# Performance work log

Measured on AMD Instinct MI355X. Metric: run time of the kernel, lower is better.

Reference implementation:

```python
import jax, jax.numpy as jnp
import numpy as np

N = 8192; E = 131072; K = 20; IN_DIM = 3; HID = 256; N_CLASSES = 32


def setup_inputs():
    key = jax.random.key(0)
    ks = jax.random.split(key, 16)

    def w(k, shape):
        lim = 1.0 / np.sqrt(shape[0])
        return jax.random.uniform(k, shape, jnp.float32, -lim, lim)

    f32 = jnp.float32
    return {
        "features": jax.random.normal(ks[0], (N, IN_DIM), f32),
        "src": jax.random.randint(ks[1], (E,), 0, N, jnp.int32),
        "dst": jax.random.randint(ks[2], (E,), 0, N, jnp.int32),
        # GraphConv params
        "Wc1": w(ks[3], (IN_DIM, HID)), "bc1": jnp.zeros((HID,), f32),
        "Wc2": w(ks[4], (HID, HID)), "bc2": jnp.zeros((HID,), f32),
        "Wc3": w(ks[5], (64, N_CLASSES)), "bc3": jnp.zeros((N_CLASSES,), f32),
        # DynamicEdgeConv 1 MLP: [2*256 -> 256 -> 256], Linear+BN+ReLU each
        "W11": w(ks[6], (2 * HID, 256)), "b11": jnp.zeros((256,), f32), "g11": jnp.ones((256,), f32), "be11": jnp.zeros((256,), f32),
        "W12": w(ks[7], (256, 256)), "b12": jnp.zeros((256,), f32), "g12": jnp.ones((256,), f32), "be12": jnp.zeros((256,), f32),
        # DynamicEdgeConv 2 MLP: [2*256 -> 64 -> 64]
        "W21": w(ks[8], (2 * 256, 64)), "b21": jnp.zeros((64,), f32), "g21": jnp.ones((64,), f32), "be21": jnp.zeros((64,), f32),
        "W22": w(ks[9], (64, 64)), "b22": jnp.zeros((64,), f32), "g22": jnp.ones((64,), f32), "be22": jnp.zeros((64,), f32),
    }


def reference(features, src, dst, Wc1, bc1, Wc2, bc2, Wc3, bc3,
              W11, b11, g11, be11, W12, b12, g12, be12,
              W21, b21, g21, be21, W22, b22, g22, be22):
    n = features.shape[0]
    ones_e = jnp.ones(src.shape[0], features.dtype)
    # DGL GraphConv norm='both': deg clamped to min 1
    dout = jnp.clip(jax.ops.segment_sum(ones_e, src, num_segments=n), 1.0) ** -0.5
    din = jnp.clip(jax.ops.segment_sum(ones_e, dst, num_segments=n), 1.0) ** -0.5

    def gconv(x, W, b, act):
        agg = jax.ops.segment_sum((x * dout[:, None])[src], dst, num_segments=n)
        r = (agg * din[:, None]) @ W + b
        return jax.nn.relu(r) if act else r

    def bn(x, g, b):  # BatchNorm1d in training mode over all edge rows
        mu = jnp.mean(x, axis=(0, 1), keepdims=True)
        var = jnp.mean(jnp.square(x - mu), axis=(0, 1), keepdims=True)
        return (x - mu) * jax.lax.rsqrt(var + 1e-5) * g + b

    def edge_conv(x, layers):
        # dynamic kNN graph on current features (self included, dist 0)
        sq = jnp.sum(x * x, axis=-1)
        d = sq[:, None] + sq[None, :] - 2.0 * (x @ x.T)  # [N,N]
        idx = jax.lax.top_k(-d, K)[1]                    # [N,K]
        xi = x[:, None, :]
        e = jnp.concatenate([jnp.broadcast_to(xi, (n, K, x.shape[-1])), x[idx] - xi], axis=-1)  # [N,K,2F]
        for W, b, g, be in layers:
            e = jax.nn.relu(bn(e @ W + b, g, be))
        return jnp.max(e, axis=1)  # max aggregation over neighbors

    h = gconv(features, Wc1, bc1, True)                                   # [N,256]
    h = edge_conv(h, [(W11, b11, g11, be11), (W12, b12, g12, be12)])      # [N,256]
    h = gconv(h, Wc2, bc2, True)                                          # [N,256]
    h = edge_conv(h, [(W21, b21, g21, be21), (W22, b22, g22, be22)])      # [N,64]
    return gconv(h, Wc3, bc3, False)                                      # [N,32]
```

## Files before the change

### kernel.cpp

```cpp
#include <hip/hip_runtime.h>

#define NN 8192
#define NE 131072
#define KNN 20
#define CH 4096
#define GBM 128
#define GBN 128
#define GBK 64

typedef __attribute__((ext_vector_type(4))) float f32x4;
typedef __attribute__((ext_vector_type(8))) __bf16 bf16x8;

__global__ void k_zero(float* p, int n){
  int i = blockIdx.x*256 + threadIdx.x;
  if (i < n) p[i] = 0.f;
}
__global__ void k_zero_i(int* p, int n){
  int i = blockIdx.x*256 + threadIdx.x;
  if (i < n) p[i] = 0;
}

__device__ __forceinline__ unsigned short f2bf(float x){
  unsigned u = __float_as_uint(x);
  unsigned r = (u + 0x7fff + ((u >> 16) & 1)) >> 16;
  return (unsigned short)r;
}
__device__ __forceinline__ float bf2f(unsigned short h){
  return __uint_as_float((unsigned)h << 16);
}
__device__ __forceinline__ void gload16(const void* g, void* l){
  __builtin_amdgcn_global_load_lds(
      (const __attribute__((address_space(1))) void*)g,
      (__attribute__((address_space(3))) void*)l, 16, 0, 0);
}

__global__ void k_count(const int* __restrict__ src, const int* __restrict__ dst,
                        int* cs, int* cd){
  int e = blockIdx.x*256 + threadIdx.x;
  if (e < NE){ atomicAdd(&cs[src[e]], 1); atomicAdd(&cd[dst[e]], 1); }
}
__global__ void k_deg(const int* cs, const int* cd, float* dout, float* din){
  int i = blockIdx.x*256 + threadIdx.x;
  if (i < NN){
    dout[i] = rsqrtf((float)max(cs[i], 1));
    din[i]  = rsqrtf((float)max(cd[i], 1));
  }
}
__global__ void k_scan(const int* __restrict__ cnt, int* __restrict__ off){
  __shared__ int sh[256];
  __shared__ int carry;
  int tid = threadIdx.x;
  if (tid == 0) carry = 0;
  __syncthreads();
  for (int base = 0; base < NN; base += 256){
    int v = cnt[base + tid];
    int x = v;
    sh[tid] = x; __syncthreads();
    for (int o = 1; o < 256; o <<= 1){
      int y = (tid >= o) ? sh[tid - o] : 0;
      __syncthreads();
      x += y; sh[tid] = x;
      __syncthreads();
    }
    off[base + tid] = carry + x - v;
    __syncthreads();
    if (tid == 255){
      carry += x;
      if (base + 256 == NN) off[NN] = carry;
    }
    __syncthreads();
  }
}
__global__ void k_fill(const int* __restrict__ src, const int* __restrict__ dst,
                       const int* __restrict__ roff, int* cursor, int* csr){
  int e = blockIdx.x*256 + threadIdx.x;
  if (e < NE){
    int d = dst[e];
    int p = atomicAdd(&cursor[d], 1);
    csr[roff[d] + p] = src[e];
  }
}

__global__ void k_gconv1(const float* __restrict__ feat, const int* __restrict__ roff,
                         const int* __restrict__ csr, const float* __restrict__ dout,
                         const float* __restrict__ din, const float* __restrict__ Wc1,
                         const float* __restrict__ bc1, float* __restrict__ h1){
  int wid = threadIdx.x >> 6, lane = threadIdx.x & 63;
  int i = blockIdx.x*4 + wid;
  float a0=0.f, a1=0.f, a2=0.f;
  int beg = roff[i], end = roff[i+1];
  for (int t = beg + lane; t < end; t += 64){
    int s = csr[t]; float w = dout[s];
    a0 += feat[s*3+0]*w; a1 += feat[s*3+1]*w; a2 += feat[s*3+2]*w;
  }
  for (int m = 32; m; m >>= 1){
    a0 += __shfl_xor(a0, m); a1 += __shfl_xor(a1, m); a2 += __shfl_xor(a2, m);
  }
  float dn = din[i];
  a0 *= dn; a1 *= dn; a2 *= dn;
  for (int c = lane; c < 256; c += 64){
    float r = a0*Wc1[c] + a1*Wc1[256+c] + a2*Wc1[512+c] + bc1[c];
    h1[(size_t)i*256 + c] = fmaxf(r, 0.f);
  }
}

__global__ void k_sq(const float* __restrict__ X, float* __restrict__ sq){
  int wid = threadIdx.x >> 6, lane = threadIdx.x & 63;
  int i = blockIdx.x*4 + wid;
  float4 v = *(const float4*)&X[(size_t)i*256 + lane*4];
  float s = v.x*v.x + v.y*v.y + v.z*v.z + v.w*v.w;
  for (int m = 32; m; m >>= 1) s += __shfl_xor(s, m);
  if (lane == 0) sq[i] = s;
}

__global__ void k_split(const float* __restrict__ X, unsigned short* __restrict__ xcat){
  int row = blockIdx.x, c = threadIdx.x;
  float x = X[(size_t)row*256 + c];
  unsigned short h = f2bf(x);
  unsigned short lo = f2bf(x - bf2f(h));
  xcat[(size_t)row*512 + c] = h;
  xcat[(size_t)row*512 + 256 + c] = lo;
}

__global__ void k_wsplit(const float* __restrict__ W, unsigned short* __restrict__ Whi,
                         unsigned short* __restrict__ Wlo){
  int k = blockIdx.x, n = threadIdx.x;
  float x = W[(size_t)k*256 + n];
  unsigned short h = f2bf(x);
  Whi[(size_t)n*256 + k] = h;
  Wlo[(size_t)n*256 + k] = f2bf(x - bf2f(h));
}

__global__ __launch_bounds__(256)
void k_gram_mfma(const unsigned short* __restrict__ Xcat,
                 float* __restrict__ G, int r0){
  __shared__ unsigned short sA[GBM*GBK];
  __shared__ unsigned short sB[GBM*GBK];
  int tid = threadIdx.x;
  int lw = tid >> 6, l = tid & 63;
  int rbl = blockIdx.y*GBM;
  int rb = r0 + rbl;
  int cb = blockIdx.x*GBN;

  int srow = l >> 3;
  int scol = (l & 7) ^ srow;
  const unsigned short* srcA[4];
  const unsigned short* srcB[4];
  char* dstA[4]; char* dstB[4];
  #pragma unroll
  for (int i = 0; i < 4; i++){
    int c = lw*4 + i;
    int row = c*8 + srow;
    srcA[i] = Xcat + (size_t)(rb + row)*512 + scol*8;
    srcB[i] = Xcat + (size_t)(cb + row)*512 + scol*8;
    dstA[i] = (char*)sA + c*1024;
    dstB[i] = (char*)sB + c*1024;
  }

  int wm = lw >> 1, wn = lw & 1;
  int fm = l & 15, kg = l >> 4;
  unsigned offA[4][2], offB[4][2];
  #pragma unroll
  for (int mf = 0; mf < 4; mf++){
    int rowa = wm*64 + mf*16 + fm;
    int rowb = wn*64 + mf*16 + fm;
    #pragma unroll
    for (int ks = 0; ks < 2; ks++){
      offA[mf][ks] = rowa*128 + (((unsigned)(ks*4 + kg) ^ (rowa & 7)))*16;
      offB[mf][ks] = rowb*128 + (((unsigned)(ks*4 + kg) ^ (rowb & 7)))*16;
    }
  }

  f32x4 acc[4][4];
  #pragma unroll
  for (int m = 0; m < 4; m++)
    #pragma unroll
    for (int n = 0; n < 4; n++) acc[m][n] = (f32x4){0.f,0.f,0.f,0.f};

  #pragma unroll
  for (int s = 0; s < 12; s++){
    int sec = s >> 2;
    int inner = (s & 3)*64;
    int cbA = (sec == 1 ? 256 : 0) + inner;
    int cbB = (sec == 2 ? 256 : 0) + inner;
    #pragma unroll
    for (int i = 0; i < 4; i++){
      gload16(srcA[i] + cbA, dstA[i]);
      gload16(srcB[i] + cbB, dstB[i]);
    }
    __syncthreads();
    #pragma unroll
    for (int ks = 0; ks < 2; ks++){
      bf16x8 a[4], b[4];
      #pragma unroll
      for (int mf = 0; mf < 4; mf++) a[mf] = *(const bf16x8*)((const char*)sA + offA[mf][ks]);
      #pragma unroll
      for (int nf = 0; nf < 4; nf++) b[nf] = *(const bf16x8*)((const char*)sB + offB[nf][ks]);
      #pragma unroll
      for (int mf = 0; mf < 4; mf++)
        #pragma unroll
        for (int nf = 0; nf < 4; nf++)
          acc[mf][nf] = __builtin_amdgcn_mfma_f32_16x16x32_bf16(a[mf], b[nf], acc[mf][nf], 0, 0, 0);
    }
    __syncthreads();
  }

  #pragma unroll
  for (int mf = 0; mf < 4; mf++){
    int orow = rbl + wm*64 + mf*16 + kg*4;
    #pragma unroll
    for (int nf = 0; nf < 4; nf++){
      int ocol = cb + wn*64 + nf*16 + fm;
      #pragma unroll
      for (int r = 0; r < 4; r++)
        G[(size_t)(orow + r)*NN + ocol] = acc[mf][nf][r];
    }
  }
}

__global__ __launch_bounds__(256)
void k_topk(const float* __restrict__ G, const float* __restrict__ sq,
            int r0, int* __restrict__ idxo){
  __shared__ float lsq[NN];
  int tid = threadIdx.x;
  for (int t = tid; t < NN/4; t += 256)
    ((float4*)lsq)[t] = ((const float4*)sq)[t];
  __syncthreads();

  int wid = tid >> 6, lane = tid & 63;
  int rl = blockIdx.x*4 + wid;
  int gr = r0 + rl;
  const float4* row4 = (const float4*)(G + (size_t)rl*NN);
  const float4* lsq4 = (const float4*)lsq;
  float sqr = lsq[gr];

  float kd0=INFINITY,kd1=INFINITY,kd2=INFINITY,kd3=INFINITY,kd4=INFINITY,
        kd5=INFINITY,kd6=INFINITY,kd7=INFINITY,kd8=INFINITY,kd9=INFINITY,
        kd10=INFINITY,kd11=INFINITY,kd12=INFINITY,kd13=INFINITY,kd14=INFINITY,
        kd15=INFINITY,kd16=INFINITY,kd17=INFINITY,kd18=INFINITY,kd19=INFINITY;
  int ki0=0x7fffffff,ki1=0x7fffffff,ki2=0x7fffffff,ki3=0x7fffffff,ki4=0x7fffffff,
      ki5=0x7fffffff,ki6=0x7fffffff,ki7=0x7fffffff,ki8=0x7fffffff,ki9=0x7fffffff,
      ki10=0x7fffffff,ki11=0x7fffffff,ki12=0x7fffffff,ki13=0x7fffffff,ki14=0x7fffffff,
      ki15=0x7fffffff,ki16=0x7fffffff,ki17=0x7fffffff,ki18=0x7fffffff,ki19=0x7fffffff;

#define ST(U) { bool sw = nk < kd##U; float tv = kd##U; int tq = ki##U; \
      if (sw){ kd##U = nk; ki##U = ni; nk = tv; ni = tq; } }
#define INSE(kc, jc) { if ((kc) < kd19){ float nk = (kc); int ni = (jc); \
      ST(0) ST(1) ST(2) ST(3) ST(4) ST(5) ST(6) ST(7) ST(8) ST(9) \
      ST(10) ST(11) ST(12) ST(13) ST(14) ST(15) ST(16) ST(17) ST(18) ST(19) } }

  #pragma unroll 1
  for (int o = 0; o < 32; o++){
    int t4 = lane + o*64;
    float4 g = row4[t4];
    float4 s = lsq4[t4];
    int jb = t4*4;
    float k0 = (sqr + s.x) - 2.f*g.x;
    float k1 = (sqr + s.y) - 2.f*g.y;
    float k2 = (sqr + s.z) - 2.f*g.z;
    float k3 = (sqr + s.w) - 2.f*g.w;
    float t19 = kd19;
    float mn = fminf(fminf(k0,k1), fminf(k2,k3));
    if (__any(mn < t19)){
      INSE(k0, jb+0);
      INSE(k1, jb+1);
      INSE(k2, jb+2);
      INSE(k3, jb+3);
    }
  }
#undef INSE
#undef ST

#define MV(A,B) { kd##A = kd##B; ki##A = ki##B; }
  #pragma unroll 1
  for (int r = 0; r < KNN; r++){
    float bv = kd0; int bi = ki0;
    #pragma unroll
    for (int mm = 32; mm; mm >>= 1){
      float ov = __shfl_xor(bv, mm); int oi = __shfl_xor(bi, mm);
      if (ov < bv || (ov == bv && oi < bi)){ bv = ov; bi = oi; }
    }
    if (ki0 == bi){
      MV(0,1) MV(1,2) MV(2,3) MV(3,4) MV(4,5) MV(5,6) MV(6,7) MV(7,8) MV(8,9) MV(9,10)
      MV(10,11) MV(11,12) MV(12,13) MV(13,14) MV(14,15) MV(15,16) MV(16,17) MV(17,18) MV(18,19)
      kd19 = INFINITY; ki19 = 0x7fffffff;
    }
    if (lane == 0) idxo[(size_t)gr*KNN + r] = bi;
  }
#undef MV
}

__global__ void k_wd(const float* __restrict__ W, float* __restrict__ Wd, int rows, int M){
  int t = blockIdx.x*256 + threadIdx.x;
  if (t < rows*M) Wd[t] = W[t] - W[rows*M + t];
}

__global__ __launch_bounds__(256)
void k_mm(const float* __restrict__ A, const float* __restrict__ B,
          const float* __restrict__ bias, float* __restrict__ Cout,
          int n, int Kd, int M, int relu){
  __shared__ float la[16][68], lb[16][68];
  int tid = threadIdx.x;
  int rb = blockIdx.y*64, cb = blockIdx.x*64;
  int lr = tid >> 2, lq = (tid & 3)*4;
  int ty = tid >> 4, tx = tid & 15;
  float acc[4][4] = {};
  for (int k0 = 0; k0 < Kd; k0 += 16){
    __syncthreads();
    #pragma unroll
    for (int u = 0; u < 4; u++){
      int k = k0 + lq + u;
      la[lq+u][lr] = (k < Kd) ? A[(size_t)(rb+lr)*Kd + k] : 0.f;
    }
    int kk = tid >> 4; int cc = (tid & 15)*4;
    #pragma unroll
    for (int u = 0; u < 4; u++){
      int c = cb + cc + u; int k = k0 + kk;
      lb[kk][cc+u] = (k < Kd && c < M) ? B[(size_t)k*M + c] : 0.f;
    }
    __syncthreads();
    #pragma unroll
    for (int k = 0; k < 16; k++){
      float4 a = *(const float4*)&la[k][ty*4];
      float4 b = *(const float4*)&lb[k][tx*4];
      float avv[4] = {a.x,a.y,a.z,a.w}, bvv[4] = {b.x,b.y,b.z,b.w};
      #pragma unroll
      for (int u = 0; u < 4; u++)
        #pragma unroll
        for (int v = 0; v < 4; v++) acc[u][v] += avv[u]*bvv[v];
    }
  }
  #pragma unroll
  for (int u = 0; u < 4; u++){
    int r = rb + ty*4 + u;
    #pragma unroll
    for (int v = 0; v < 4; v++){
      int c = cb + tx*4 + v;
      if (c < M){
        float x = acc[u][v] + (bias ? bias[c] : 0.f);
        if (relu) x = fmaxf(x, 0.f);
        Cout[(size_t)r*M + c] = x;
      }
    }
  }
}

template<int C>
__global__ __launch_bounds__(256)
void k_stats1(const float* __restrict__ A, const float* __restrict__ P,
              const int* __restrict__ idx, float* __restrict__ ssum, float* __restrict__ ssq){
  __shared__ int si[128], sj[128];
  int tid = threadIdx.x;
  int s0 = blockIdx.x*128;
  if (tid < 128){ si[tid] = (s0 + tid)/KNN; sj[tid] = idx[s0 + tid]; }
  __syncthreads();
  constexpr int MPAR = 256/C;
  int tc = tid % C, sr = tid / C;
  float s = 0.f, q = 0.f;
  for (int m = sr; m < 128; m += MPAR){
    float v = A[(size_t)si[m]*C + tc] + P[(size_t)sj[m]*C + tc];
    s += v; q += v*v;
  }
  if constexpr (MPAR > 1){
    __shared__ float rs[256], rq[256];
    rs[tid] = s; rq[tid] = q; __syncthreads();
    if (sr == 0){
      for (int u = 1; u < MPAR; u++){ s += rs[u*C + tc]; q += rq[u*C + tc]; }
    }
  }
  if (sr == 0){ atomicAdd(&ssum[tc], s); atomicAdd(&ssq[tc], q); }
}

template<int C>
__global__ __launch_bounds__(256)
void k_colstats(const float* __restrict__ X, float* __restrict__ ssum, float* __restrict__ ssq){
  constexpr int MPAR = 256/C;
  int tid = threadIdx.x;
  int tc = tid % C, sr = tid / C;
  int base = blockIdx.x*256;
  float s = 0.f, q = 0.f;
  for (int m = sr; m < 256; m += MPAR){
    float v = X[(size_t)(base + m)*C + tc];
    s += v; q += v*v;
  }
  if constexpr (MPAR > 1){
    __shared__ float rs[256], rq[256];
    rs[tid] = s; rq[tid] = q; __syncthreads();
    if (sr == 0){
      for (int u = 1; u < MPAR; u++){ s += rs[u*C + tc]; q += rq[u*C + tc]; }
    }
  }
  if (sr == 0){ atomicAdd(&ssum[tc], s); atomicAdd(&ssq[tc], q); }
}

__global__ void k_bn_final(const float* __restrict__ ssum, const float* __restrict__ ssq,
                           const float* __restrict__ g, const float* __restrict__ be,
                           float* __restrict__ sb, float* __restrict__ tb, int C, float invn){
  int c = threadIdx.x;
  if (c < C){
    float mu = ssum[c]*invn;
    float var = fmaxf(ssq[c]*invn - mu*mu, 0.f);
    float s = g[c]*rsqrtf(var + 1e-5f);
    sb[c] = s; tb[c] = be[c] - mu*s;
  }
}

__global__ __launch_bounds__(256, 2)
void k_edge_mfma(const float* __restrict__ A, const float* __restrict__ P,
                 const int* __restrict__ idx, const float* __restrict__ sb,
                 const float* __restrict__ tb, const unsigned short* __restrict__ Wthi,
                 const unsigned short* __restrict__ Wtlo, const float* __restrict__ bias,
                 float* __restrict__ out){
  __shared__ unsigned short ehi[64*256];
  __shared__ unsigned short elo[64*256];
  __shared__ int sj[64];
  int tid = threadIdx.x;
  int lw = tid >> 6, l = tid & 63;
  int s0 = blockIdx.x*64;
  if (tid < 64) sj[tid] = idx[s0 + tid];
  float sbc = sb[tid], tbc = tb[tid];
  __syncthreads();

  #pragma unroll 1
  for (int it = 0; it < 64; it++){
    int i = (s0 + it)/KNN;
    int j = sj[it];
    float v = (A[(size_t)i*256 + tid] + P[(size_t)j*256 + tid])*sbc + tbc;
    v = fmaxf(v, 0.f);
    unsigned short h = f2bf(v);
    unsigned short lo = f2bf(v - bf2f(h));
    unsigned off = (unsigned)it*512 + (((unsigned)tid*2) ^ (((unsigned)it & 7) << 4));
    *(unsigned short*)((char*)ehi + off) = h;
    *(unsigned short*)((char*)elo + off) = lo;
  }
  __syncthreads();

  int fm = l & 15, kg = l >> 4;
  const unsigned short* bhi[4];
  const unsigned short* blo[4];
  float bz[4];
  #pragma unroll
  for (int nf = 0; nf < 4; nf++){
    int col = lw*64 + nf*16 + fm;
    bhi[nf] = Wthi + (size_t)col*256 + kg*8;
    blo[nf] = Wtlo + (size_t)col*256 + kg*8;
    bz[nf] = bias[col];
  }

  f32x4 acc[4][4];
  #pragma unroll
  for (int m = 0; m < 4; m++)
    #pragma unroll
    for (int n = 0; n < 4; n++) acc[m][n] = (f32x4){0.f,0.f,0.f,0.f};

  #pragma unroll 1
  for (int sec = 0; sec < 3; sec++){
    const char* abase = (sec == 1) ? (const char*)elo : (const char*)ehi;
    int bsec = (sec == 2);
    #pragma unroll 1
    for (int st = 0; st < 8; st++){
      int g = st*4 + kg;
      bf16x8 a[4], b[4];
      #pragma unroll
      for (int mf = 0; mf < 4; mf++){
        int row = mf*16 + fm;
        a[mf] = *(const bf16x8*)(abase + row*512 + ((unsigned)(g ^ (row & 7)))*16);
      }
      #pragma unroll
      for (int nf = 0; nf < 4; nf++){
        const unsigned short* bp = bsec ? blo[nf] : bhi[nf];
        b[nf] = *(const bf16x8*)(bp + st*32);
      }
      #pragma unroll
      for (int mf = 0; mf < 4; mf++)
        #pragma unroll
        for (int nf = 0; nf < 4; nf++)
          acc[mf][nf] = __builtin_amdgcn_mfma_f32_16x16x32_bf16(a[mf], b[nf], acc[mf][nf], 0, 0, 0);
    }
  }

  #pragma unroll
  for (int mf = 0; mf < 4; mf++){
    #pragma unroll
    for (int nf = 0; nf < 4; nf++){
      int col = lw*64 + nf*16 + fm;
      #pragma unroll
      for (int r = 0; r < 4; r++){
        int row = s0 + mf*16 + kg*4 + r;
        out[(size_t)row*256 + col] = acc[mf][nf][r] + bz[nf];
      }
    }
  }
}

template<int C>
__global__ __launch_bounds__(256)
void k_edge_mm(const float* __restrict__ A, const float* __restrict__ P,
               const int* __restrict__ idx, const float* __restrict__ sb,
               const float* __restrict__ tb, const float* __restrict__ W,
               const float* __restrict__ bias, float* __restrict__ out){
  constexpr int BM   = (C == 256) ? 32 : 64;
  constexpr int KT   = (C == 256) ? 16 : 64;
  constexpr int COLG = C/8;
  constexpr int ROWG = 256/COLG;
  constexpr int EPT  = BM/ROWG;
  constexpr int MPAR = 256/C;
  __shared__ float e2[BM][C+1];
  __shared__ float wt[KT][C+4];
  __shared__ int sj[BM];
  int tid = threadIdx.x;
  int s0 = blockIdx.x*BM;
  if (tid < BM) sj[tid] = idx[s0 + tid];
  __syncthreads();
  for (int mb = 0; mb < BM; mb += MPAR){
    int m = mb + tid / C;
    int c = tid % C;
    int i = (s0 + m)/KNN;
    int j = sj[m];
    float v = (A[(size_t)i*C + c] + P[(size_t)j*C + c])*sb[c] + tb[c];
    e2[m][c] = fmaxf(v, 0.f);
  }
  float acc[EPT][8];
  #pragma unroll
  for (int m = 0; m < EPT; m++)
    #pragma unroll
    for (int u = 0; u < 8; u++) acc[m][u] = 0.f;
  int tr = tid / COLG, tc = tid % COLG;
  for (int kt = 0; kt < C; kt += KT){
    __syncthreads();
    for (int t = tid; t < KT*C; t += 256){
      wt[t / C][t % C] = W[(size_t)(kt + t/C)*C + (t % C)];
    }
    __syncthreads();
    #pragma unroll 4
    for (int k = 0; k < KT; k++){
      float4 w0 = *(const float4*)&wt[k][tc*8];
      float4 w1 = *(const float4*)&wt[k][tc*8 + 4];
      float b[8] = {w0.x,w0.y,w0.z,w0.w,w1.x,w1.y,w1.z,w1.w};
      #pragma unroll
      for (int m = 0; m < EPT; m++){
        float a = e2[tr*EPT + m][kt + k];
        #pragma unroll
        for (int u = 0; u < 8; u++) acc[m][u] += a*b[u];
      }
    }
  }
  #pragma unroll
  for (int m = 0; m < EPT; m++){
    int row = s0 + tr*EPT + m;
    float4 o0, o1;
    o0.x = acc[m][0] + bias[tc*8+0]; o0.y = acc[m][1] + bias[tc*8+1];
    o0.z = acc[m][2] + bias[tc*8+2]; o0.w = acc[m][3] + bias[tc*8+3];
    o1.x = acc[m][4] + bias[tc*8+4]; o1.y = acc[m][5] + bias[tc*8+5];
    o1.z = acc[m][6] + bias[tc*8+6]; o1.w = acc[m][7] + bias[tc*8+7];
    *(float4*)&out[(size_t)row*C + tc*8]     = o0;
    *(float4*)&out[(size_t)row*C + tc*8 + 4] = o1;
  }
}

template<int C>
__global__ void k_maxpool(const float* __restrict__ X, const float* __restrict__ sb,
                          const float* __restrict__ tb, float* __restrict__ H){
  constexpr int NPB = 256/C;
  int node = blockIdx.x*NPB + threadIdx.x / C;
  int c = threadIdx.x % C;
  float s = sb[c], t = tb[c];
  float mx = 0.f;
  for (int k = 0; k < KNN; k++){
    float v = X[(size_t)(node*KNN + k)*C + c]*s + t;
    mx = fmaxf(mx, v);
  }
  H[(size_t)node*C + c] = mx;
}

template<int C>
__global__ void k_agg(const float* __restrict__ X, const int* __restrict__ roff,
                      const int* __restrict__ csr, const float* __restrict__ dout,
                      const float* __restrict__ din, float* __restrict__ XA){
  int i = blockIdx.x; int c = threadIdx.x;
  float acc = 0.f;
  int b = roff[i], e = roff[i+1];
  for (int t = b; t < e; t++){
    int s = csr[t];
    acc += X[(size_t)s*C + c]*dout[s];
  }
  XA[(size_t)i*C + c] = acc*din[i];
}

extern "C" void kernel_launch(void* const* d_in, const int* in_sizes, int n_in,
                              void* d_out, int out_size, void* d_ws, size_t ws_size,
                              hipStream_t stream){
  const float* feat = (const float*)d_in[0];
  const int*   src  = (const int*)d_in[1];
  const int*   dst  = (const int*)d_in[2];
  const float* Wc1  = (const float*)d_in[3];
  const float* bc1  = (const float*)d_in[4];
  const float* Wc2  = (const float*)d_in[5];
  const float* bc2  = (const float*)d_in[6];
  const float* Wc3  = (const float*)d_in[7];
  const float* bc3  = (const float*)d_in[8];
  const float* W11  = (const float*)d_in[9];
  const float* b11  = (const float*)d_in[10];
  const float* g11  = (const float*)d_in[11];
  const float* be11 = (const float*)d_in[12];
  const float* W12  = (const float*)d_in[13];
  const float* b12  = (const float*)d_in[14];
  const float* g12  = (const float*)d_in[15];
  const float* be12 = (const float*)d_in[16];
  const float* W21  = (const float*)d_in[17];
  const float* b21  = (const float*)d_in[18];
  const float* g21  = (const float*)d_in[19];
  const float* be21 = (const float*)d_in[20];
  const float* W22  = (const float*)d_in[21];
  const float* b22  = (const float*)d_in[22];
  const float* g22  = (const float*)d_in[23];
  const float* be22 = (const float*)d_in[24];
  float* out = (float*)d_out;

  char* w = (char*)d_ws; size_t off = 0;
  auto alloc = [&](size_t bytes)->void*{
    void* p = w + off;
    off += bytes; off = (off + 255) & ~(size_t)255;
    return p;
  };
  int* cnt_s  = (int*)alloc(NN*4);
  int* cnt_d  = (int*)alloc(NN*4);
  int* roff   = (int*)alloc((NN+1)*4);
  int* cursor = (int*)alloc(NN*4);
  int* csr    = (int*)alloc(NE*4);
  int* idx    = (int*)alloc((size_t)NN*KNN*4);
  float* dout = (float*)alloc(NN*4);
  float* din  = (float*)alloc(NN*4);
  float* sqv  = (float*)alloc(NN*4);
  float* h1   = (float*)alloc((size_t)NN*256*4);
  float* h2   = (float*)alloc((size_t)NN*256*4);
  float* h3   = (float*)alloc((size_t)NN*256*4);
  float* h4   = (float*)alloc((size_t)NN*64*4);
  float* xa   = (float*)alloc((size_t)NN*256*4);
  float* Abuf = (float*)alloc((size_t)NN*256*4);
  float* Pbuf = (float*)alloc((size_t)NN*256*4);
  float* Wd   = (float*)alloc(256*256*4);
  float* ssum = (float*)alloc(256*4);
  float* ssq  = (float*)alloc(256*4);
  float* sbn  = (float*)alloc(256*4);
  float* tbn  = (float*)alloc(256*4);
  unsigned short* wthi = (unsigned short*)alloc(256*256*2);
  unsigned short* wtlo = (unsigned short*)alloc(256*256*2);
  float* out2 = (float*)alloc((size_t)NN*KNN*256*4);
  float* gram = out2;
  unsigned short* xcat = (unsigned short*)(out2 + (size_t)CH*NN);
  (void)ws_size; (void)n_in; (void)in_sizes; (void)out_size;

  const float invn = 1.0f / (float)(NN*KNN);

  k_zero_i<<<32, 256, 0, stream>>>(cnt_s, NN);
  k_zero_i<<<32, 256, 0, stream>>>(cnt_d, NN);
  k_zero_i<<<32, 256, 0, stream>>>(cursor, NN);
  k_count<<<NE/256, 256, 0, stream>>>(src, dst, cnt_s, cnt_d);
  k_deg<<<32, 256, 0, stream>>>(cnt_s, cnt_d, dout, din);
  k_scan<<<1, 256, 0, stream>>>(cnt_d, roff);
  k_fill<<<NE/256, 256, 0, stream>>>(src, dst, roff, cursor, csr);

  k_gconv1<<<NN/4, 256, 0, stream>>>(feat, roff, csr, dout, din, Wc1, bc1, h1);

  k_sq<<<NN/4, 256, 0, stream>>>(h1, sqv);
  k_split<<<NN, 256, 0, stream>>>(h1, xcat);
  for (int r0 = 0; r0 < NN; r0 += CH){
    k_gram_mfma<<<dim3(NN/GBN, CH/GBM), 256, 0, stream>>>(xcat, gram, r0);
    k_topk<<<CH/4, 256, 0, stream>>>(gram, sqv, r0, idx);
  }
  k_wd<<<256, 256, 0, stream>>>(W11, Wd, 256, 256);
  k_wsplit<<<256, 256, 0, stream>>>(W12, wthi, wtlo);
  k_mm<<<dim3(4, NN/64), 256, 0, stream>>>(h1, Wd, b11, Abuf, NN, 256, 256, 0);
  k_mm<<<dim3(4, NN/64), 256, 0, stream>>>(h1, W11 + 256*256, nullptr, Pbuf, NN, 256, 256, 0);
  k_zero<<<2, 256, 0, stream>>>(ssum, 256); k_zero<<<2, 256, 0, stream>>>(ssq, 256);
  k_stats1<256><<<NN*KNN/128, 256, 0, stream>>>(Abuf, Pbuf, idx, ssum, ssq);
  k_bn_final<<<1, 256, 0, stream>>>(ssum, ssq, g11, be11, sbn, tbn, 256, invn);
  k_edge_mfma<<<NN*KNN/64, 256, 0, stream>>>(Abuf, Pbuf, idx, sbn, tbn, wthi, wtlo, b12, out2);
  k_zero<<<2, 256, 0, stream>>>(ssum, 256); k_zero<<<2, 256, 0, stream>>>(ssq, 256);
  k_colstats<256><<<NN*KNN/256, 256, 0, stream>>>(out2, ssum, ssq);
  k_bn_final<<<1, 256, 0, stream>>>(ssum, ssq, g12, be12, sbn, tbn, 256, invn);
  k_maxpool<256><<<NN, 256, 0, stream>>>(out2, sbn, tbn, h2);

  k_agg<256><<<NN, 256, 0, stream>>>(h2, roff, csr, dout, din, xa);
  k_mm<<<dim3(4, NN/64), 256, 0, stream>>>(xa, Wc2, bc2, h3, NN, 256, 256, 1);

  k_sq<<<NN/4, 256, 0, stream>>>(h3, sqv);
  k_split<<<NN, 256, 0, stream>>>(h3, xcat);
  for (int r0 = 0; r0 < NN; r0 += CH){
    k_gram_mfma<<<dim3(NN/GBN, CH/GBM), 256, 0, stream>>>(xcat, gram, r0);
    k_topk<<<CH/4, 256, 0, stream>>>(gram, sqv, r0, idx);
  }
  k_wd<<<64, 256, 0, stream>>>(W21, Wd, 256, 64);
  k_mm<<<dim3(1, NN/64), 256, 0, stream>>>(h3, Wd, b21, Abuf, NN, 256, 64, 0);
  k_mm<<<dim3(1, NN/64), 256, 0, stream>>>(h3, W21 + 256*64, nullptr, Pbuf, NN, 256, 64, 0);
  k_zero<<<2, 256, 0, stream>>>(ssum, 256); k_zero<<<2, 256, 0, stream>>>(ssq, 256);
  k_stats1<64><<<NN*KNN/128, 256, 0, stream>>>(Abuf, Pbuf, idx, ssum, ssq);
  k_bn_final<<<1, 256, 0, stream>>>(ssum, ssq, g21, be21, sbn, tbn, 64, invn);
  k_edge_mm<64><<<NN*KNN/64, 256, 0, stream>>>(Abuf, Pbuf, idx, sbn, tbn, W22, b22, out2);
  k_zero<<<2, 256, 0, stream>>>(ssum, 256); k_zero<<<2, 256, 0, stream>>>(ssq, 256);
  k_colstats<64><<<NN*KNN/256, 256, 0, stream>>>(out2, ssum, ssq);
  k_bn_final<<<1, 256, 0, stream>>>(ssum, ssq, g22, be22, sbn, tbn, 64, invn);
  k_maxpool<64><<<NN/4, 256, 0, stream>>>(out2, sbn, tbn, h4);

  k_agg<64><<<NN, 64, 0, stream>>>(h4, roff, csr, dout, din, xa);
  k_mm<<<dim3(1, NN/64), 256, 0, stream>>>(xa, Wc3, bc3, out, NN, 64, 32, 0);
}
```

Measured before the change: 1.462 ms.

## Fuse BN column stats into edge GEMMs and move 64-wide edge MLP to MFMA

```diff
diff --git a/kernel.cpp b/kernel.cpp
--- a/kernel.cpp
+++ b/kernel.cpp
@@ -130,6 +130,14 @@
   Whi[(size_t)n*256 + k] = h;
   Wlo[(size_t)n*256 + k] = f2bf(x - bf2f(h));
 }
+__global__ void k_wsplit64(const float* __restrict__ W, unsigned short* __restrict__ Whi,
+                           unsigned short* __restrict__ Wlo){
+  int k = blockIdx.x, n = threadIdx.x;
+  float x = W[(size_t)k*64 + n];
+  unsigned short h = f2bf(x);
+  Whi[(size_t)n*64 + k] = h;
+  Wlo[(size_t)n*64 + k] = f2bf(x - bf2f(h));
+}
 
 __global__ __launch_bounds__(256)
 void k_gram_mfma(const unsigned short* __restrict__ Xcat,
@@ -249,12 +257,16 @@
       ST(0) ST(1) ST(2) ST(3) ST(4) ST(5) ST(6) ST(7) ST(8) ST(9) \
       ST(10) ST(11) ST(12) ST(13) ST(14) ST(15) ST(16) ST(17) ST(18) ST(19) } }
 
+  float4 gc = row4[lane];
+  float4 sc = lsq4[lane];
   #pragma unroll 1
   for (int o = 0; o < 32; o++){
-    int t4 = lane + o*64;
-    float4 g = row4[t4];
-    float4 s = lsq4[t4];
-    int jb = t4*4;
+    float4 g = gc, s = sc;
+    if (o < 31){
+      gc = row4[lane + (o+1)*64];
+      sc = lsq4[lane + (o+1)*64];
+    }
+    int jb = (lane + o*64)*4;
     float k0 = (sqr + s.x) - 2.f*g.x;
     float k1 = (sqr + s.y) - 2.f*g.y;
     float k2 = (sqr + s.z) - 2.f*g.z;
@@ -371,28 +383,6 @@
   if (sr == 0){ atomicAdd(&ssum[tc], s); atomicAdd(&ssq[tc], q); }
 }
 
-template<int C>
-__global__ __launch_bounds__(256)
-void k_colstats(const float* __restrict__ X, float* __restrict__ ssum, float* __restrict__ ssq){
-  constexpr int MPAR = 256/C;
-  int tid = threadIdx.x;
-  int tc = tid % C, sr = tid / C;
-  int base = blockIdx.x*256;
-  float s = 0.f, q = 0.f;
-  for (int m = sr; m < 256; m += MPAR){
-    float v = X[(size_t)(base + m)*C + tc];
-    s += v; q += v*v;
-  }
-  if constexpr (MPAR > 1){
-    __shared__ float rs[256], rq[256];
-    rs[tid] = s; rq[tid] = q; __syncthreads();
-    if (sr == 0){
-      for (int u = 1; u < MPAR; u++){ s += rs[u*C + tc]; q += rq[u*C + tc]; }
-    }
-  }
-  if (sr == 0){ atomicAdd(&ssum[tc], s); atomicAdd(&ssq[tc], q); }
-}
-
 __global__ void k_bn_final(const float* __restrict__ ssum, const float* __restrict__ ssq,
                            const float* __restrict__ g, const float* __restrict__ be,
                            float* __restrict__ sb, float* __restrict__ tb, int C, float invn){
@@ -410,7 +400,7 @@
                  const int* __restrict__ idx, const float* __restrict__ sb,
                  const float* __restrict__ tb, const unsigned short* __restrict__ Wthi,
                  const unsigned short* __restrict__ Wtlo, const float* __restrict__ bias,
-                 float* __restrict__ out){
+                 float* __restrict__ out, float* __restrict__ ssum, float* __restrict__ ssq){
   __shared__ unsigned short ehi[64*256];
   __shared__ unsigned short elo[64*256];
   __shared__ int sj[64];
@@ -422,16 +412,25 @@
   __syncthreads();
 
   #pragma unroll 1
-  for (int it = 0; it < 64; it++){
-    int i = (s0 + it)/KNN;
-    int j = sj[it];
-    float v = (A[(size_t)i*256 + tid] + P[(size_t)j*256 + tid])*sbc + tbc;
-    v = fmaxf(v, 0.f);
-    unsigned short h = f2bf(v);
-    unsigned short lo = f2bf(v - bf2f(h));
-    unsigned off = (unsigned)it*512 + (((unsigned)tid*2) ^ (((unsigned)it & 7) << 4));
-    *(unsigned short*)((char*)ehi + off) = h;
-    *(unsigned short*)((char*)elo + off) = lo;
+  for (int g = 0; g < 8; g++){
+    float va[8];
+    #pragma unroll
+    for (int u = 0; u < 8; u++){
+      int it = g*8 + u;
+      int i = (s0 + it)/KNN;
+      int j = sj[it];
+      va[u] = A[(size_t)i*256 + tid] + P[(size_t)j*256 + tid];
+    }
+    #pragma unroll
+    for (int u = 0; u < 8; u++){
+      int it = g*8 + u;
+      float v = fmaxf(va[u]*sbc + tbc, 0.f);
+      unsigned short h = f2bf(v);
+      unsigned short lo = f2bf(v - bf2f(h));
+      unsigned off = (unsigned)it*512 + (((unsigned)tid*2) ^ (((unsigned)it & 7) << 4));
+      *(unsigned short*)((char*)ehi + off) = h;
+      *(unsigned short*)((char*)elo + off) = lo;
+    }
   }
   __syncthreads();
 
@@ -479,6 +478,9 @@
     }
   }
 
+  float s4[4], q4[4];
+  #pragma unroll
+  for (int nf = 0; nf < 4; nf++){ s4[nf] = 0.f; q4[nf] = 0.f; }
   #pragma unroll
   for (int mf = 0; mf < 4; mf++){
     #pragma unroll
@@ -487,74 +489,141 @@
       #pragma unroll
       for (int r = 0; r < 4; r++){
         int row = s0 + mf*16 + kg*4 + r;
-        out[(size_t)row*256 + col] = acc[mf][nf][r] + bz[nf];
+        float v = acc[mf][nf][r] + bz[nf];
+        out[(size_t)row*256 + col] = v;
+        s4[nf] += v; q4[nf] += v*v;
       }
     }
   }
-}
-
-template<int C>
-__global__ __launch_bounds__(256)
-void k_edge_mm(const float* __restrict__ A, const float* __restrict__ P,
-               const int* __restrict__ idx, const float* __restrict__ sb,
-               const float* __restrict__ tb, const float* __restrict__ W,
-               const float* __restrict__ bias, float* __restrict__ out){
-  constexpr int BM   = (C == 256) ? 32 : 64;
-  constexpr int KT   = (C == 256) ? 16 : 64;
-  constexpr int COLG = C/8;
-  constexpr int ROWG = 256/COLG;
-  constexpr int EPT  = BM/ROWG;
-  constexpr int MPAR = 256/C;
-  __shared__ float e2[BM][C+1];
-  __shared__ float wt[KT][C+4];
-  __shared__ int sj[BM];
+  #pragma unroll
+  for (int nf = 0; nf < 4; nf++){
+    s4[nf] += __shfl_xor(s4[nf], 16); q4[nf] += __shfl_xor(q4[nf], 16);
+    s4[nf] += __shfl_xor(s4[nf], 32); q4[nf] += __shfl_xor(q4[nf], 32);
+  }
+  if (kg == 0){
+    #pragma unroll
+    for (int nf = 0; nf < 4; nf++){
+      int col = lw*64 + nf*16 + fm;
+      atomicAdd(&ssum[col], s4[nf]);
+      atomicAdd(&ssq[col], q4[nf]);
+    }
+  }
+}
+
+__global__ __launch_bounds__(256, 2)
+void k_edge_mfma64(const float* __restrict__ A, const float* __restrict__ P,
+                   const int* __restrict__ idx, const float* __restrict__ sb,
+                   const float* __restrict__ tb, const unsigned short* __restrict__ Wthi,
+                   const unsigned short* __restrict__ Wtlo, const float* __restrict__ bias,
+                   float* __restrict__ out, float* __restrict__ ssum, float* __restrict__ ssq){
+  __shared__ unsigned short ehi[128*64];
+  __shared__ unsigned short elo[128*64];
+  __shared__ int sj[128];
   int tid = threadIdx.x;
-  int s0 = blockIdx.x*BM;
-  if (tid < BM) sj[tid] = idx[s0 + tid];
+  int lw = tid >> 6, l = tid & 63;
+  int s0 = blockIdx.x*128;
+  if (tid < 128) sj[tid] = idx[s0 + tid];
+  int col0 = tid & 63, rgrp = tid >> 6;
+  float sbc = sb[col0], tbc = tb[col0];
   __syncthreads();
-  for (int mb = 0; mb < BM; mb += MPAR){
-    int m = mb + tid / C;
-    int c = tid % C;
-    int i = (s0 + m)/KNN;
-    int j = sj[m];
-    float v = (A[(size_t)i*C + c] + P[(size_t)j*C + c])*sb[c] + tb[c];
-    e2[m][c] = fmaxf(v, 0.f);
-  }
-  float acc[EPT][8];
-  #pragma unroll
-  for (int m = 0; m < EPT; m++)
-    #pragma unroll
-    for (int u = 0; u < 8; u++) acc[m][u] = 0.f;
-  int tr = tid / COLG, tc = tid % COLG;
-  for (int kt = 0; kt < C; kt += KT){
-    __syncthreads();
-    for (int t = tid; t < KT*C; t += 256){
-      wt[t / C][t % C] = W[(size_t)(kt + t/C)*C + (t % C)];
-    }
-    __syncthreads();
-    #pragma unroll 4
-    for (int k = 0; k < KT; k++){
-      float4 w0 = *(const float4*)&wt[k][tc*8];
-      float4 w1 = *(const float4*)&wt[k][tc*8 + 4];
-      float b[8] = {w0.x,w0.y,w0.z,w0.w,w1.x,w1.y,w1.z,w1.w};
-      #pragma unroll
-      for (int m = 0; m < EPT; m++){
-        float a = e2[tr*EPT + m][kt + k];
+
+  #pragma unroll 1
+  for (int g = 0; g < 4; g++){
+    float va[8];
+    #pragma unroll
+    for (int u = 0; u < 8; u++){
+      int it = (g*8 + u)*4 + rgrp;
+      int i = (s0 + it)/KNN;
+      int j = sj[it];
+      va[u] = A[(size_t)i*64 + col0] + P[(size_t)j*64 + col0];
+    }
+    #pragma unroll
+    for (int u = 0; u < 8; u++){
+      int it = (g*8 + u)*4 + rgrp;
+      float v = fmaxf(va[u]*sbc + tbc, 0.f);
+      unsigned short h = f2bf(v);
+      unsigned short lo = f2bf(v - bf2f(h));
+      unsigned off = (unsigned)it*128 + (((unsigned)col0*2) ^ (((unsigned)it & 7) << 4));
+      *(unsigned short*)((char*)ehi + off) = h;
+      *(unsigned short*)((char*)elo + off) = lo;
+    }
+  }
+  __syncthreads();
+
+  int wm = lw >> 1, wn = lw & 1;
+  int fm = l & 15, kg = l >> 4;
+  const unsigned short* bhi[2];
+  const unsigned short* blo[2];
+  float bz[2];
+  #pragma unroll
+  for (int nf = 0; nf < 2; nf++){
+    int col = wn*32 + nf*16 + fm;
+    bhi[nf] = Wthi + (size_t)col*64 + kg*8;
+    blo[nf] = Wtlo + (size_t)col*64 + kg*8;
+    bz[nf] = bias[col];
+  }
+
+  f32x4 acc[4][2];
+  #pragma unroll
+  for (int m = 0; m < 4; m++)
+    #pragma unroll
+    for (int n = 0; n < 2; n++) acc[m][n] = (f32x4){0.f,0.f,0.f,0.f};
+
+  #pragma unroll 1
+  for (int sec = 0; sec < 3; sec++){
+    const char* abase = (sec == 1) ? (const char*)elo : (const char*)ehi;
+    int bsec = (sec == 2);
+    #pragma unroll
+    for (int ks = 0; ks < 2; ks++){
+      int g = ks*4 + kg;
+      bf16x8 a[4], b[2];
+      #pragma unroll
+      for (int mf = 0; mf < 4; mf++){
+        int row = wm*64 + mf*16 + fm;
+        a[mf] = *(const bf16x8*)(abase + row*128 + ((unsigned)(g ^ (row & 7)))*16);
+      }
+      #pragma unroll
+      for (int nf = 0; nf < 2; nf++){
+        const unsigned short* bp = bsec ? blo[nf] : bhi[nf];
+        b[nf] = *(const bf16x8*)(bp + ks*32);
+      }
+      #pragma unroll
+      for (int mf = 0; mf < 4; mf++)
         #pragma unroll
-        for (int u = 0; u < 8; u++) acc[m][u] += a*b[u];
+        for (int nf = 0; nf < 2; nf++)
+          acc[mf][nf] = __builtin_amdgcn_mfma_f32_16x16x32_bf16(a[mf], b[nf], acc[mf][nf], 0, 0, 0);
+    }
+  }
+
+  float s2[2], q2[2];
+  #pragma unroll
+  for (int nf = 0; nf < 2; nf++){ s2[nf] = 0.f; q2[nf] = 0.f; }
+  #pragma unroll
+  for (int mf = 0; mf < 4; mf++){
+    #pragma unroll
+    for (int nf = 0; nf < 2; nf++){
+      int col = wn*32 + nf*16 + fm;
+      #pragma unroll
+      for (int r = 0; r < 4; r++){
+        int row = s0 + wm*64 + mf*16 + kg*4 + r;
+        float v = acc[mf][nf][r] + bz[nf];
+        out[(size_t)row*64 + col] = v;
+        s2[nf] += v; q2[nf] += v*v;
       }
     }
   }
   #pragma unroll
-  for (int m = 0; m < EPT; m++){
-    int row = s0 + tr*EPT + m;
-    float4 o0, o1;
-    o0.x = acc[m][0] + bias[tc*8+0]; o0.y = acc[m][1] + bias[tc*8+1];
-    o0.z = acc[m][2] + bias[tc*8+2]; o0.w = acc[m][3] + bias[tc*8+3];
-    o1.x = acc[m][4] + bias[tc*8+4]; o1.y = acc[m][5] + bias[tc*8+5];
-    o1.z = acc[m][6] + bias[tc*8+6]; o1.w = acc[m][7] + bias[tc*8+7];
-    *(float4*)&out[(size_t)row*C + tc*8]     = o0;
-    *(float4*)&out[(size_t)row*C + tc*8 + 4] = o1;
+  for (int nf = 0; nf < 2; nf++){
+    s2[nf] += __shfl_xor(s2[nf], 16); q2[nf] += __shfl_xor(q2[nf], 16);
+    s2[nf] += __shfl_xor(s2[nf], 32); q2[nf] += __shfl_xor(q2[nf], 32);
+  }
+  if (kg == 0){
+    #pragma unroll
+    for (int nf = 0; nf < 2; nf++){
+      int col = wn*32 + nf*16 + fm;
+      atomicAdd(&ssum[col], s2[nf]);
+      atomicAdd(&ssq[col], q2[nf]);
+    }
   }
 }
 
@@ -646,6 +715,8 @@
   float* tbn  = (float*)alloc(256*4);
   unsigned short* wthi = (unsigned short*)alloc(256*256*2);
   unsigned short* wtlo = (unsigned short*)alloc(256*256*2);
+  unsigned short* w64hi = (unsigned short*)alloc(64*64*2);
+  unsigned short* w64lo = (unsigned short*)alloc(64*64*2);
   float* out2 = (float*)alloc((size_t)NN*KNN*256*4);
   float* gram = out2;
   unsigned short* xcat = (unsigned short*)(out2 + (size_t)CH*NN);
@@ -676,9 +747,8 @@
   k_zero<<<2, 256, 0, stream>>>(ssum, 256); k_zero<<<2, 256, 0, stream>>>(ssq, 256);
   k_stats1<256><<<NN*KNN/128, 256, 0, stream>>>(Abuf, Pbuf, idx, ssum, ssq);
   k_bn_final<<<1, 256, 0, stream>>>(ssum, ssq, g11, be11, sbn, tbn, 256, invn);
-  k_edge_mfma<<<NN*KNN/64, 256, 0, stream>>>(Abuf, Pbuf, idx, sbn, tbn, wthi, wtlo, b12, out2);
   k_zero<<<2, 256, 0, stream>>>(ssum, 256); k_zero<<<2, 256, 0, stream>>>(ssq, 256);
-  k_colstats<256><<<NN*KNN/256, 256, 0, stream>>>(out2, ssum, ssq);
+  k_edge_mfma<<<NN*KNN/64, 256, 0, stream>>>(Abuf, Pbuf, idx, sbn, tbn, wthi, wtlo, b12, out2, ssum, ssq);
   k_bn_final<<<1, 256, 0, stream>>>(ssum, ssq, g12, be12, sbn, tbn, 256, invn);
   k_maxpool<256><<<NN, 256, 0, stream>>>(out2, sbn, tbn, h2);
 
@@ -692,14 +762,14 @@
     k_topk<<<CH/4, 256, 0, stream>>>(gram, sqv, r0, idx);
   }
   k_wd<<<64, 256, 0, stream>>>(W21, Wd, 256, 64);
+  k_wsplit64<<<64, 64, 0, stream>>>(W22, w64hi, w64lo);
   k_mm<<<dim3(1, NN/64), 256, 0, stream>>>(h3, Wd, b21, Abuf, NN, 256, 64, 0);
   k_mm<<<dim3(1, NN/64), 256, 0, stream>>>(h3, W21 + 256*64, nullptr, Pbuf, NN, 256, 64, 0);
   k_zero<<<2, 256, 0, stream>>>(ssum, 256); k_zero<<<2, 256, 0, stream>>>(ssq, 256);
   k_stats1<64><<<NN*KNN/128, 256, 0, stream>>>(Abuf, Pbuf, idx, ssum, ssq);
   k_bn_final<<<1, 256, 0, stream>>>(ssum, ssq, g21, be21, sbn, tbn, 64, invn);
-  k_edge_mm<64><<<NN*KNN/64, 256, 0, stream>>>(Abuf, Pbuf, idx, sbn, tbn, W22, b22, out2);
   k_zero<<<2, 256, 0, stream>>>(ssum, 256); k_zero<<<2, 256, 0, stream>>>(ssq, 256);
-  k_colstats<64><<<NN*KNN/256, 256, 0, stream>>>(out2, ssum, ssq);
+  k_edge_mfma64<<<NN*KNN/128, 256, 0, stream>>>(Abuf, Pbuf, idx, sbn, tbn, w64hi, w64lo, b22, out2, ssum, ssq);
   k_bn_final<<<1, 256, 0, stream>>>(ssum, ssq, g22, be22, sbn, tbn, 64, invn);
   k_maxpool<64><<<NN/4, 256, 0, stream>>>(out2, sbn, tbn, h4);
 
```

Result: faster. 1.393 ms (-4.7%).
